# Kernel optimization log

Hardware: AMD Instinct MI355X
Metric: run time of the kernel (lower is better)

Reference implementation:

```python
import jax, jax.numpy as jnp
import numpy as np

B, C, L, H, D = 2, 1024, 2048, 16, 64  # batch, n_factor, seq, heads, head_dim
LN_EPS = 1e-5


def setup_inputs() -> dict:
    key = jax.random.key(0)
    ks = jax.random.split(key, 8)
    s = 0.02
    return {
        "x": jax.random.normal(ks[0], (B, C, L), jnp.float32),
        "y": jax.random.normal(ks[1], (B, C, L), jnp.float32),
        "Wq": jax.random.normal(ks[2], (H, C, D), jnp.float32) * s,
        "Wk": jax.random.normal(ks[3], (H, C, D), jnp.float32) * s,
        "Wv": jax.random.normal(ks[4], (H, C, D), jnp.float32) * s,
        "bq": jax.random.normal(ks[5], (H, D), jnp.float32) * s,
        "bk": jax.random.normal(ks[6], (H, D), jnp.float32) * s,
        "bv": jax.random.normal(ks[7], (H, D), jnp.float32) * s,
        "gamma": jnp.ones((C,), jnp.float32),
        "beta": jnp.zeros((C,), jnp.float32),
    }


def reference(x, y, Wq, Wk, Wv, bq, bk, bv, gamma, beta):
    # Per-head Conv1d(kernel=1) == per-position linear; batch all heads at once.
    # x,y: [B, C, L]; W*: [H, C, D]; result q/k/v: [B, H, L, D]
    q = jnp.einsum('bcl,hcd->bhld', x, Wq) + bq[None, :, None, :]
    k = jnp.einsum('bcl,hcd->bhld', y, Wk) + bk[None, :, None, :]
    v = jnp.einsum('bcl,hcd->bhld', y, Wv) + bv[None, :, None, :]

    scale = 1.0 / jnp.sqrt(jnp.float32(D))  # n_factor_head ** 0.5
    scores = jnp.einsum('bhqd,bhkd->bhqk', q, k) * scale  # [B,H,L,L]
    attn = jax.nn.softmax(scores, axis=-1)
    ctx = jnp.einsum('bhqk,bhkd->bhqd', attn, v)  # [B,H,L,D]

    # torch.cat over heads along last dim == [B, L, H*D]
    att = jnp.transpose(ctx, (0, 2, 1, 3)).reshape(B, L, H * D)

    h = jnp.transpose(x, (0, 2, 1)) + att  # residual on x permuted to [B,L,C]
    mu = jnp.mean(h, axis=-1, keepdims=True)
    var = jnp.var(h, axis=-1, keepdims=True)
    out = (h - mu) * jax.lax.rsqrt(var + LN_EPS) * gamma + beta
    # dropout: identity in eval mode
    return out
```

## Files before the change

### kernel.cpp

```cpp
#include <hip/hip_runtime.h>
#include <hip/hip_bf16.h>

#define DEVI __device__ __forceinline__

typedef unsigned short u16;
typedef __bf16 bf16x8 __attribute__((ext_vector_type(8)));
typedef float f32x4 __attribute__((ext_vector_type(4)));

constexpr int Bn = 2, Cn = 1024, Ln = 2048, Hn = 16, Dn = 64;

DEVI u16 f2bfu(float f) { return __builtin_bit_cast(u16, __float2bfloat16(f)); }
DEVI float bfu2f(u16 u) { return __bfloat162float(__builtin_bit_cast(__hip_bfloat16, u)); }
DEVI f32x4 mfma16(bf16x8 a, bf16x8 b, f32x4 c) {
  return __builtin_amdgcn_mfma_f32_16x16x32_bf16(a, b, c, 0, 0, 0);
}
DEVI unsigned pk2(float lo, float hi) {
  return (unsigned)f2bfu(lo) | ((unsigned)f2bfu(hi) << 16);
}
DEVI void gld16(const u16* g, u16* l) {
  __builtin_amdgcn_global_load_lds(
      (const __attribute__((address_space(1))) unsigned*)g,
      (__attribute__((address_space(3))) unsigned*)l, 16, 0, 0);
}

__global__ __launch_bounds__(256) void transpose_xy(const float* __restrict__ x,
                                                    const float* __restrict__ y,
                                                    u16* __restrict__ xT,
                                                    u16* __restrict__ yT) {
  int z = blockIdx.z;
  int which = z >> 1, b = z & 1;
  const float* src = (which ? y : x) + (size_t)b * Cn * Ln;
  u16* dst = (which ? yT : xT) + (size_t)b * Ln * Cn;
  int l0 = blockIdx.x * 64, c0 = blockIdx.y * 64;
  __shared__ float tile[64][65];
  int t = threadIdx.x;
  #pragma unroll
  for (int i = 0; i < 16; ++i) {
    int idx = i * 256 + t;
    int r = idx >> 6, cc = idx & 63;
    tile[r][cc] = src[(size_t)(c0 + r) * Ln + (l0 + cc)];
  }
  __syncthreads();
  #pragma unroll
  for (int i = 0; i < 8; ++i) {
    int idx = i * 256 + t;
    int r = idx >> 5, cc = (idx & 31) * 2;
    unsigned pkv = pk2(tile[cc][r], tile[cc + 1][r]);
    *(unsigned*)(&dst[(size_t)(l0 + r) * Cn + (c0 + cc)]) = pkv;
  }
}

__global__ __launch_bounds__(256) void transpose_w(const float* __restrict__ Wq,
                                                   const float* __restrict__ Wk,
                                                   const float* __restrict__ Wv,
                                                   u16* __restrict__ WT) {
  int c0 = blockIdx.x * 64, h = blockIdx.y, which = blockIdx.z;
  const float* src = (which == 0 ? Wq : (which == 1 ? Wk : Wv)) + (size_t)h * Cn * Dn;
  u16* dst = WT + ((size_t)which * Hn + h) * Dn * Cn;
  __shared__ float tile[64][65];
  int t = threadIdx.x;
  #pragma unroll
  for (int i = 0; i < 16; ++i) {
    int idx = i * 256 + t;
    int r = idx >> 6, cc = idx & 63;
    tile[r][cc] = src[(size_t)(c0 + r) * Dn + cc];
  }
  __syncthreads();
  #pragma unroll
  for (int i = 0; i < 16; ++i) {
    int idx = i * 256 + t;
    int r = idx >> 6, cc = idx & 63;
    dst[(size_t)r * Cn + (c0 + cc)] = f2bfu(tile[cc][r]);
  }
}

__global__ __launch_bounds__(256) void gemm_qkv3(const u16* __restrict__ xT,
                                                 const u16* __restrict__ yT,
                                                 const u16* __restrict__ WT,
                                                 const float* __restrict__ bq,
                                                 const float* __restrict__ bk,
                                                 const float* __restrict__ bv,
                                                 u16* __restrict__ Qb,
                                                 u16* __restrict__ Kb,
                                                 u16* __restrict__ Vt) {
  int mt = blockIdx.x, by = blockIdx.y, b = blockIdx.z;
  int which = by >> 3, hp = by & 7;
  const u16* A = (which == 0 ? xT : yT) + (size_t)b * Ln * Cn + (size_t)mt * 128 * Cn;
  const u16* Bw = WT + ((size_t)which * 1024 + (size_t)hp * 128) * Cn;
  __shared__ __align__(16) u16 smem[2 * 128 * 64];
  u16* lA = smem;
  u16* lB = smem + 128 * 64;
  int t = threadIdx.x, wave = t >> 6, lane = t & 63;
  int wr = wave >> 1, wc = wave & 1;
  int ml = lane & 15, kg = lane >> 4;
  f32x4 acc[4][4] = {};
  for (int k0 = 0; k0 < Cn; k0 += 64) {
    __syncthreads();
    #pragma unroll
    for (int j = 0; j < 4; ++j) {
      int q = wave * 256 + j * 64 + lane;
      int row = q >> 3, p = q & 7, c16 = p ^ (row & 7);
      gld16(A + (size_t)row * Cn + k0 + c16 * 8, &lA[(wave * 256 + j * 64) * 8]);
    }
    #pragma unroll
    for (int j = 0; j < 4; ++j) {
      int q = wave * 256 + j * 64 + lane;
      int row = q >> 3, p = q & 7, c16 = p ^ (row & 7);
      gld16(Bw + (size_t)row * Cn + k0 + c16 * 8, &lB[(wave * 256 + j * 64) * 8]);
    }
    __syncthreads();
    bf16x8 af[4][2], bf[4][2];
    #pragma unroll
    for (int m = 0; m < 4; ++m) {
      int row = wr * 64 + m * 16 + ml;
      #pragma unroll
      for (int kk = 0; kk < 2; ++kk) {
        int p = (kk * 4 + kg) ^ (row & 7);
        af[m][kk] = *(const bf16x8*)(&lA[row * 64 + p * 8]);
      }
    }
    #pragma unroll
    for (int n = 0; n < 4; ++n) {
      int row = wc * 64 + n * 16 + ml;
      #pragma unroll
      for (int kk = 0; kk < 2; ++kk) {
        int p = (kk * 4 + kg) ^ (row & 7);
        bf[n][kk] = *(const bf16x8*)(&lB[row * 64 + p * 8]);
      }
    }
    #pragma unroll
    for (int m = 0; m < 4; ++m)
      #pragma unroll
      for (int n = 0; n < 4; ++n)
        #pragma unroll
        for (int kk = 0; kk < 2; ++kk)
          acc[m][n] = mfma16(af[m][kk], bf[n][kk], acc[m][n]);
  }
  int head = hp * 2 + wc;
  const float* bp = (which == 0 ? bq : (which == 1 ? bk : bv));
  if (which < 2) {
    u16* O = (which == 0 ? Qb : Kb) + (((size_t)b * Hn + head) * Ln + (size_t)mt * 128) * Dn;
    #pragma unroll
    for (int n = 0; n < 4; ++n) {
      float bvv = bp[head * 64 + n * 16 + ml];
      #pragma unroll
      for (int m = 0; m < 4; ++m)
        #pragma unroll
        for (int r = 0; r < 4; ++r) {
          int row = wr * 64 + m * 16 + kg * 4 + r;
          O[(size_t)row * Dn + n * 16 + ml] = f2bfu(acc[m][n][r] + bvv);
        }
    }
  } else {
    __syncthreads();
    #pragma unroll
    for (int n = 0; n < 4; ++n) {
      float bvv = bp[head * 64 + n * 16 + ml];
      int n_loc = wc * 64 + n * 16 + ml;
      int swz = (n_loc & 7) << 4;
      #pragma unroll
      for (int m = 0; m < 4; ++m) {
        int m_base = wr * 64 + m * 16 + kg * 4;
        uint2 pkd;
        pkd.x = pk2(acc[m][n][0] + bvv, acc[m][n][1] + bvv);
        pkd.y = pk2(acc[m][n][2] + bvv, acc[m][n][3] + bvv);
        *(uint2*)(&smem[n_loc * 128 + (m_base ^ swz)]) = pkd;
      }
    }
    __syncthreads();
    u16* Vbase = Vt + ((size_t)b * Hn + hp * 2) * Dn * Ln + (size_t)mt * 128;
    #pragma unroll
    for (int i = 0; i < 8; ++i) {
      int chunk = i * 256 + t;
      int n = chunk >> 4, cc = chunk & 15;
      uint4 vv = *(const uint4*)(&smem[n * 128 + (cc ^ ((n & 7) << 1)) * 8]);
      *(uint4*)(Vbase + (size_t)n * Ln + cc * 8) = vv;
    }
  }
}

__global__ __launch_bounds__(256) void flash_attn(const u16* __restrict__ Qg,
                                                  const u16* __restrict__ Kg,
                                                  const u16* __restrict__ Vtg,
                                                  float* __restrict__ att) {
  int qt = blockIdx.x, h = blockIdx.y, b = blockIdx.z;
  size_t bh = (size_t)b * Hn + h;
  const u16* Qp = Qg + (bh * Ln + (size_t)qt * 64) * Dn;
  const u16* Kp = Kg + bh * Ln * Dn;
  const u16* Vp = Vtg + bh * Dn * Ln;
  int t = threadIdx.x, wave = t >> 6, lane = t & 63;
  int ml = lane & 15, kg = lane >> 4, mlx = ml & 7;
  __shared__ __align__(16) u16 Kl[2][64 * 64];
  __shared__ __align__(16) u16 Vl[2][64 * 64];
  __shared__ __align__(16) u16 Pl[4][16 * 64];
  u16* Pw = Pl[wave];

  constexpr float QS = 0.125f * 1.44269504f;
  bf16x8 qf[2];
  #pragma unroll
  for (int kk = 0; kk < 2; ++kk) {
    bf16x8 raw = *(const bf16x8*)(Qp + (size_t)(wave * 16 + ml) * Dn + kk * 32 + kg * 8);
    #pragma unroll
    for (int j = 0; j < 8; ++j) raw[j] = (__bf16)((float)raw[j] * QS);
    qf[kk] = raw;
  }

  f32x4 ctx[4] = {};
  float psum = 0.f;

  auto stage = [&](int buf, int kv0) {
    #pragma unroll
    for (int j = 0; j < 2; ++j) {
      int q = wave * 128 + j * 64 + lane;
      int row = q >> 3, p = q & 7, c16 = p ^ (row & 7);
      gld16(Kp + (size_t)(kv0 + row) * Dn + c16 * 8, &Kl[buf][(wave * 128 + j * 64) * 8]);
    }
    #pragma unroll
    for (int j = 0; j < 2; ++j) {
      int q = wave * 128 + j * 64 + lane;
      int row = q >> 3, p = q & 7, c16 = p ^ (row & 7);
      gld16(Vp + (size_t)row * Ln + kv0 + c16 * 8, &Vl[buf][(wave * 128 + j * 64) * 8]);
    }
  };

  stage(0, 0);
  __syncthreads();

  constexpr int NT = Ln / 64;
  for (int tt = 0; tt < NT; ++tt) {
    int cur = tt & 1;
    if (tt + 1 < NT) stage(cur ^ 1, (tt + 1) * 64);
    const u16* Kh = Kl[cur];
    const u16* Vh = Vl[cur];
    f32x4 s[4] = {};
    #pragma unroll
    for (int nt = 0; nt < 4; ++nt) {
      int row = nt * 16 + ml;
      #pragma unroll
      for (int kk = 0; kk < 2; ++kk) {
        int p = (kk * 4 + kg) ^ mlx;
        bf16x8 kf = *(const bf16x8*)(&Kh[row * 64 + p * 8]);
        s[nt] = mfma16(kf, qf[kk], s[nt]);
      }
    }
    #pragma unroll
    for (int nt = 0; nt < 4; ++nt) {
      f32x4 e;
      #pragma unroll
      for (int r = 0; r < 4; ++r) e[r] = __builtin_amdgcn_exp2f(s[nt][r]);
      psum += (e[0] + e[1]) + (e[2] + e[3]);
      uint2 pkd;
      pkd.x = pk2(e[0], e[1]);
      pkd.y = pk2(e[2], e[3]);
      int chunk = (nt * 2 + (kg >> 1)) ^ mlx;
      *(uint2*)(&Pw[ml * 64 + chunk * 8 + (kg & 1) * 4]) = pkd;
    }
    bf16x8 pf[2];
    #pragma unroll
    for (int kk = 0; kk < 2; ++kk) {
      int c = (kk * 4 + kg) ^ mlx;
      pf[kk] = *(const bf16x8*)(&Pw[ml * 64 + c * 8]);
    }
    #pragma unroll
    for (int nt = 0; nt < 4; ++nt) {
      int row = nt * 16 + ml;
      #pragma unroll
      for (int kk = 0; kk < 2; ++kk) {
        int p = (kk * 4 + kg) ^ mlx;
        bf16x8 vf = *(const bf16x8*)(&Vh[row * 64 + p * 8]);
        ctx[nt] = mfma16(pf[kk], vf, ctx[nt]);
      }
    }
    if (tt + 1 < NT) __syncthreads();
  }
  psum += __shfl_xor(psum, 16);
  psum += __shfl_xor(psum, 32);
  float inv[4];
  #pragma unroll
  for (int r = 0; r < 4; ++r) inv[r] = 1.f / __shfl(psum, kg * 4 + r);
  #pragma unroll
  for (int nt = 0; nt < 4; ++nt)
    #pragma unroll
    for (int r = 0; r < 4; ++r) {
      size_t row = (size_t)b * Ln + qt * 64 + wave * 16 + kg * 4 + r;
      att[row * Cn + h * Dn + nt * 16 + ml] = ctx[nt][r] * inv[r];
    }
}

__global__ __launch_bounds__(256) void ln_kernel(const float* __restrict__ att,
                                                 const u16* __restrict__ xT,
                                                 const float* __restrict__ gamma,
                                                 const float* __restrict__ beta,
                                                 float* __restrict__ out) {
  size_t row = blockIdx.x;
  const float* ap = att + row * Cn;
  const u16* xp = xT + row * Cn;
  float* op = out + row * Cn;
  int t = threadIdx.x;
  float4 a = *(const float4*)(ap + t * 4);
  ushort4 xv = *(const ushort4*)(xp + t * 4);
  float h0 = a.x + bfu2f(xv.x), h1 = a.y + bfu2f(xv.y);
  float h2 = a.z + bfu2f(xv.z), h3 = a.w + bfu2f(xv.w);
  float s = h0 + h1 + h2 + h3;
  float ss = h0 * h0 + h1 * h1 + h2 * h2 + h3 * h3;
  #pragma unroll
  for (int off = 1; off < 64; off <<= 1) {
    s += __shfl_xor(s, off);
    ss += __shfl_xor(ss, off);
  }
  __shared__ float red[8];
  int wave = t >> 6, lane = t & 63;
  if (lane == 0) { red[wave] = s; red[wave + 4] = ss; }
  __syncthreads();
  s = red[0] + red[1] + red[2] + red[3];
  ss = red[4] + red[5] + red[6] + red[7];
  float mu = s * (1.f / 1024.f);
  float var = ss * (1.f / 1024.f) - mu * mu;
  float rinv = rsqrtf(var + 1e-5f);
  float4 g = *(const float4*)(gamma + t * 4);
  float4 be = *(const float4*)(beta + t * 4);
  float4 o;
  o.x = (h0 - mu) * rinv * g.x + be.x;
  o.y = (h1 - mu) * rinv * g.y + be.y;
  o.z = (h2 - mu) * rinv * g.z + be.z;
  o.w = (h3 - mu) * rinv * g.w + be.w;
  *(float4*)(op + t * 4) = o;
}

extern "C" void kernel_launch(void* const* d_in, const int* in_sizes, int n_in,
                              void* d_out, int out_size, void* d_ws, size_t ws_size,
                              hipStream_t stream) {
  const float* x = (const float*)d_in[0];
  const float* y = (const float*)d_in[1];
  const float* Wq = (const float*)d_in[2];
  const float* Wk = (const float*)d_in[3];
  const float* Wv = (const float*)d_in[4];
  const float* bq = (const float*)d_in[5];
  const float* bk = (const float*)d_in[6];
  const float* bv = (const float*)d_in[7];
  const float* gamma = (const float*)d_in[8];
  const float* beta = (const float*)d_in[9];
  float* out = (float*)d_out;

  char* ws = (char*)d_ws;
  u16* xT = (u16*)(ws + 0);
  u16* yT = (u16*)(ws + 8388608);
  u16* WT = (u16*)(ws + 16777216);
  u16* Qb = (u16*)(ws + 23068672);
  u16* Kb = (u16*)(ws + 31457280);
  u16* VT = (u16*)(ws + 39845888);
  float* att = (float*)(ws + 48234496);

  transpose_xy<<<dim3(Ln / 64, Cn / 64, 4), dim3(256), 0, stream>>>(x, y, xT, yT);
  transpose_w<<<dim3(Cn / 64, Hn, 3), dim3(256), 0, stream>>>(Wq, Wk, Wv, WT);
  gemm_qkv3<<<dim3(Ln / 128, 24, Bn), dim3(256), 0, stream>>>(xT, yT, WT, bq, bk, bv, Qb, Kb, VT);
  flash_attn<<<dim3(Ln / 64, Hn, Bn), dim3(256), 0, stream>>>(Qb, Kb, VT, att);
  ln_kernel<<<dim3(Bn * Ln), dim3(256), 0, stream>>>(att, xT, gamma, beta, out);
}
```

Baseline: 127.1 us.

## Split attention KV tiles across two wave groups and store context in bf16

Flash attention now runs 512 threads per block. Two groups of four waves each take half of every 64-key tile, and their partial context and row sums are combined through shared memory at the end. This doubles the waves available to hide latency, and each wave has less work per tile. The attention output buffer is also switched from fp32 to bf16 so the layernorm kernel reads half the bytes. The cost is an extra reduction step with two barriers and lower precision in the intermediate before the residual.

```diff
diff --git a/kernel.cpp b/kernel.cpp
--- a/kernel.cpp
+++ b/kernel.cpp
@@ -179,27 +179,28 @@
   }
 }
 
-__global__ __launch_bounds__(256) void flash_attn(const u16* __restrict__ Qg,
-                                                  const u16* __restrict__ Kg,
-                                                  const u16* __restrict__ Vtg,
-                                                  float* __restrict__ att) {
+__global__ __launch_bounds__(512, 8) void flash_attn(const u16* __restrict__ Qg,
+                                                     const u16* __restrict__ Kg,
+                                                     const u16* __restrict__ Vtg,
+                                                     u16* __restrict__ att) {
   int qt = blockIdx.x, h = blockIdx.y, b = blockIdx.z;
   size_t bh = (size_t)b * Hn + h;
   const u16* Qp = Qg + (bh * Ln + (size_t)qt * 64) * Dn;
   const u16* Kp = Kg + bh * Ln * Dn;
   const u16* Vp = Vtg + bh * Dn * Ln;
   int t = threadIdx.x, wave = t >> 6, lane = t & 63;
-  int ml = lane & 15, kg = lane >> 4, mlx = ml & 7;
+  int qs = wave & 3, g = wave >> 2;
+  int ml = lane & 15, kg = lane >> 4;
   __shared__ __align__(16) u16 Kl[2][64 * 64];
   __shared__ __align__(16) u16 Vl[2][64 * 64];
-  __shared__ __align__(16) u16 Pl[4][16 * 64];
+  __shared__ __align__(16) u16 Pl[8][16 * 32];
   u16* Pw = Pl[wave];
 
   constexpr float QS = 0.125f * 1.44269504f;
   bf16x8 qf[2];
   #pragma unroll
   for (int kk = 0; kk < 2; ++kk) {
-    bf16x8 raw = *(const bf16x8*)(Qp + (size_t)(wave * 16 + ml) * Dn + kk * 32 + kg * 8);
+    bf16x8 raw = *(const bf16x8*)(Qp + (size_t)(qs * 16 + ml) * Dn + kk * 32 + kg * 8);
     #pragma unroll
     for (int j = 0; j < 8; ++j) raw[j] = (__bf16)((float)raw[j] * QS);
     qf[kk] = raw;
@@ -209,18 +210,9 @@
   float psum = 0.f;
 
   auto stage = [&](int buf, int kv0) {
-    #pragma unroll
-    for (int j = 0; j < 2; ++j) {
-      int q = wave * 128 + j * 64 + lane;
-      int row = q >> 3, p = q & 7, c16 = p ^ (row & 7);
-      gld16(Kp + (size_t)(kv0 + row) * Dn + c16 * 8, &Kl[buf][(wave * 128 + j * 64) * 8]);
-    }
-    #pragma unroll
-    for (int j = 0; j < 2; ++j) {
-      int q = wave * 128 + j * 64 + lane;
-      int row = q >> 3, p = q & 7, c16 = p ^ (row & 7);
-      gld16(Vp + (size_t)row * Ln + kv0 + c16 * 8, &Vl[buf][(wave * 128 + j * 64) * 8]);
-    }
+    int rowk = t >> 3, p = t & 7, c16 = p ^ (rowk & 7);
+    gld16(Kp + (size_t)(kv0 + rowk) * Dn + c16 * 8, &Kl[buf][wave * 512]);
+    gld16(Vp + (size_t)rowk * Ln + kv0 + c16 * 8, &Vl[buf][wave * 512]);
   };
 
   stage(0, 0);
@@ -232,19 +224,19 @@
     if (tt + 1 < NT) stage(cur ^ 1, (tt + 1) * 64);
     const u16* Kh = Kl[cur];
     const u16* Vh = Vl[cur];
-    f32x4 s[4] = {};
-    #pragma unroll
-    for (int nt = 0; nt < 4; ++nt) {
-      int row = nt * 16 + ml;
+    f32x4 s[2] = {};
+    #pragma unroll
+    for (int nt = 0; nt < 2; ++nt) {
+      int row = g * 32 + nt * 16 + ml;
       #pragma unroll
       for (int kk = 0; kk < 2; ++kk) {
-        int p = (kk * 4 + kg) ^ mlx;
+        int p = (kk * 4 + kg) ^ (row & 7);
         bf16x8 kf = *(const bf16x8*)(&Kh[row * 64 + p * 8]);
         s[nt] = mfma16(kf, qf[kk], s[nt]);
       }
     }
     #pragma unroll
-    for (int nt = 0; nt < 4; ++nt) {
+    for (int nt = 0; nt < 2; ++nt) {
       f32x4 e;
       #pragma unroll
       for (int r = 0; r < 4; ++r) e[r] = __builtin_amdgcn_exp2f(s[nt][r]);
@@ -252,55 +244,69 @@
       uint2 pkd;
       pkd.x = pk2(e[0], e[1]);
       pkd.y = pk2(e[2], e[3]);
-      int chunk = (nt * 2 + (kg >> 1)) ^ mlx;
-      *(uint2*)(&Pw[ml * 64 + chunk * 8 + (kg & 1) * 4]) = pkd;
-    }
-    bf16x8 pf[2];
-    #pragma unroll
-    for (int kk = 0; kk < 2; ++kk) {
-      int c = (kk * 4 + kg) ^ mlx;
-      pf[kk] = *(const bf16x8*)(&Pw[ml * 64 + c * 8]);
-    }
+      int chunk = (nt * 2 + (kg >> 1)) ^ (ml & 3);
+      *(uint2*)(&Pw[ml * 32 + chunk * 8 + (kg & 1) * 4]) = pkd;
+    }
+    bf16x8 pf = *(const bf16x8*)(&Pw[ml * 32 + (kg ^ (ml & 3)) * 8]);
     #pragma unroll
     for (int nt = 0; nt < 4; ++nt) {
       int row = nt * 16 + ml;
-      #pragma unroll
-      for (int kk = 0; kk < 2; ++kk) {
-        int p = (kk * 4 + kg) ^ mlx;
-        bf16x8 vf = *(const bf16x8*)(&Vh[row * 64 + p * 8]);
-        ctx[nt] = mfma16(pf[kk], vf, ctx[nt]);
-      }
+      int p = (g * 4 + kg) ^ (row & 7);
+      bf16x8 vf = *(const bf16x8*)(&Vh[row * 64 + p * 8]);
+      ctx[nt] = mfma16(pf, vf, ctx[nt]);
     }
     if (tt + 1 < NT) __syncthreads();
   }
-  psum += __shfl_xor(psum, 16);
-  psum += __shfl_xor(psum, 32);
-  float inv[4];
-  #pragma unroll
-  for (int r = 0; r < 4; ++r) inv[r] = 1.f / __shfl(psum, kg * 4 + r);
-  #pragma unroll
-  for (int nt = 0; nt < 4; ++nt)
-    #pragma unroll
-    for (int r = 0; r < 4; ++r) {
-      size_t row = (size_t)b * Ln + qt * 64 + wave * 16 + kg * 4 + r;
-      att[row * Cn + h * Dn + nt * 16 + ml] = ctx[nt][r] * inv[r];
-    }
-}
-
-__global__ __launch_bounds__(256) void ln_kernel(const float* __restrict__ att,
+  __syncthreads();
+  float* comb = (float*)&Kl[0][0];
+  float* psA = (float*)&Vl[0][0];
+  if (g == 1) {
+    int base = qs * 1024 + lane;
+    #pragma unroll
+    for (int nt = 0; nt < 4; ++nt)
+      #pragma unroll
+      for (int r = 0; r < 4; ++r)
+        comb[base + (nt * 4 + r) * 64] = ctx[nt][r];
+    psA[qs * 64 + lane] = psum;
+  }
+  __syncthreads();
+  if (g == 0) {
+    int base = qs * 1024 + lane;
+    #pragma unroll
+    for (int nt = 0; nt < 4; ++nt)
+      #pragma unroll
+      for (int r = 0; r < 4; ++r)
+        ctx[nt][r] += comb[base + (nt * 4 + r) * 64];
+    psum += psA[qs * 64 + lane];
+    psum += __shfl_xor(psum, 16);
+    psum += __shfl_xor(psum, 32);
+    float inv[4];
+    #pragma unroll
+    for (int r = 0; r < 4; ++r) inv[r] = 1.f / __shfl(psum, kg * 4 + r);
+    #pragma unroll
+    for (int nt = 0; nt < 4; ++nt)
+      #pragma unroll
+      for (int r = 0; r < 4; ++r) {
+        size_t row = (size_t)b * Ln + qt * 64 + qs * 16 + kg * 4 + r;
+        att[row * Cn + h * Dn + nt * 16 + ml] = f2bfu(ctx[nt][r] * inv[r]);
+      }
+  }
+}
+
+__global__ __launch_bounds__(256) void ln_kernel(const u16* __restrict__ att,
                                                  const u16* __restrict__ xT,
                                                  const float* __restrict__ gamma,
                                                  const float* __restrict__ beta,
                                                  float* __restrict__ out) {
   size_t row = blockIdx.x;
-  const float* ap = att + row * Cn;
+  const u16* ap = att + row * Cn;
   const u16* xp = xT + row * Cn;
   float* op = out + row * Cn;
   int t = threadIdx.x;
-  float4 a = *(const float4*)(ap + t * 4);
+  ushort4 a4 = *(const ushort4*)(ap + t * 4);
   ushort4 xv = *(const ushort4*)(xp + t * 4);
-  float h0 = a.x + bfu2f(xv.x), h1 = a.y + bfu2f(xv.y);
-  float h2 = a.z + bfu2f(xv.z), h3 = a.w + bfu2f(xv.w);
+  float h0 = bfu2f(a4.x) + bfu2f(xv.x), h1 = bfu2f(a4.y) + bfu2f(xv.y);
+  float h2 = bfu2f(a4.z) + bfu2f(xv.z), h3 = bfu2f(a4.w) + bfu2f(xv.w);
   float s = h0 + h1 + h2 + h3;
   float ss = h0 * h0 + h1 * h1 + h2 * h2 + h3 * h3;
   #pragma unroll
@@ -317,13 +323,13 @@
   float mu = s * (1.f / 1024.f);
   float var = ss * (1.f / 1024.f) - mu * mu;
   float rinv = rsqrtf(var + 1e-5f);
-  float4 g = *(const float4*)(gamma + t * 4);
-  float4 be = *(const float4*)(beta + t * 4);
+  float4 gmv = *(const float4*)(gamma + t * 4);
+  float4 bev = *(const float4*)(beta + t * 4);
   float4 o;
-  o.x = (h0 - mu) * rinv * g.x + be.x;
-  o.y = (h1 - mu) * rinv * g.y + be.y;
-  o.z = (h2 - mu) * rinv * g.z + be.z;
-  o.w = (h3 - mu) * rinv * g.w + be.w;
+  o.x = (h0 - mu) * rinv * gmv.x + bev.x;
+  o.y = (h1 - mu) * rinv * gmv.y + bev.y;
+  o.z = (h2 - mu) * rinv * gmv.z + bev.z;
+  o.w = (h3 - mu) * rinv * gmv.w + bev.w;
   *(float4*)(op + t * 4) = o;
 }
 
@@ -349,11 +355,11 @@
   u16* Qb = (u16*)(ws + 23068672);
   u16* Kb = (u16*)(ws + 31457280);
   u16* VT = (u16*)(ws + 39845888);
-  float* att = (float*)(ws + 48234496);
+  u16* att = (u16*)(ws + 48234496);
 
   transpose_xy<<<dim3(Ln / 64, Cn / 64, 4), dim3(256), 0, stream>>>(x, y, xT, yT);
   transpose_w<<<dim3(Cn / 64, Hn, 3), dim3(256), 0, stream>>>(Wq, Wk, Wv, WT);
   gemm_qkv3<<<dim3(Ln / 128, 24, Bn), dim3(256), 0, stream>>>(xT, yT, WT, bq, bk, bv, Qb, Kb, VT);
-  flash_attn<<<dim3(Ln / 64, Hn, Bn), dim3(256), 0, stream>>>(Qb, Kb, VT, att);
+  flash_attn<<<dim3(Ln / 64, Hn, Bn), dim3(512), 0, stream>>>(Qb, Kb, VT, att);
   ln_kernel<<<dim3(Bn * Ln), dim3(256), 0, stream>>>(att, xT, gamma, beta, out);
 }
```

Result: faster. 123.0 us (-3.2%).
